# Optimization experiments

Hardware: AMD Instinct MI355X
Metric: run time of the kernel (lower is better)

The kernel has to match this reference:

```python
import jax, jax.numpy as jnp
import numpy as np

B, S, DM, H, DK, R, THETA = 8, 2048, 512, 8, 64, 128, 10000.0
BLK = R          # key/query block size; window radius == block size
NB = S // BLK    # number of blocks
NEG = -1e30      # additive mask for invalid positions (fp32-safe)


def setup_inputs() -> dict:
    key = jax.random.key(0)
    ks = jax.random.split(key, 5)
    scale = 0.02
    hidden_states = jax.random.normal(ks[0], (B, S, DM), jnp.float32)
    Wq = jax.random.normal(ks[1], (DM, H * DK), jnp.float32) * scale
    Wk = jax.random.normal(ks[2], (DM, H * DK), jnp.float32) * scale
    Wv = jax.random.normal(ks[3], (DM, H * DK), jnp.float32) * scale
    Wo = jax.random.normal(ks[4], (H * DK, DM), jnp.float32) * scale
    position_ids = jnp.tile(jnp.arange(S, dtype=jnp.int64)[None, :], (B, 1))
    return {"hidden_states": hidden_states, "Wq": Wq, "Wk": Wk, "Wv": Wv,
            "Wo": Wo, "position_ids": position_ids}


def _apply_rope(q, k, position_ids):
    # q,k: [B,H,S,DK]; position_ids: [B,S]
    half = DK // 2
    inv_freq = 1.0 / (THETA ** (jnp.arange(0, DK, 2, dtype=jnp.float32) / DK))  # [half]
    freqs = position_ids.astype(jnp.float32)[:, :, None] * inv_freq[None, None, :]  # [B,S,half]
    emb = jnp.concatenate([freqs, freqs], axis=-1)        # [B,S,DK]
    cos = jnp.cos(emb)[:, None, :, :]                     # [B,1,S,DK]
    sin = jnp.sin(emb)[:, None, :, :]

    def rotate_half(x):
        return jnp.concatenate([-x[..., half:], x[..., :half]], axis=-1)

    return q * cos + rotate_half(q) * sin, k * cos + rotate_half(k) * sin


def _band_mask():
    # valid[nb, BLK, 3*BLK]: key within [0,S) and |j - i| <= R
    b = jnp.arange(NB)[:, None, None]
    qi = jnp.arange(BLK)[None, :, None]
    kj = jnp.arange(3 * BLK)[None, None, :]
    kglob = (b - 1) * BLK + kj                 # global key index
    qglob = b * BLK + qi                        # global query index
    return (jnp.abs(kglob - qglob) <= R) & (kglob >= 0) & (kglob < S)


def reference(hidden_states, Wq, Wk, Wv, Wo, position_ids):
    # projections: [B,S,DM] -> [B,H,S,DK]
    def shape(x):
        return x.reshape(B, S, H, DK).transpose(0, 2, 1, 3)

    q = shape(hidden_states @ Wq)
    k = shape(hidden_states @ Wk)
    v = shape(hidden_states @ Wv)
    q, k = _apply_rope(q, k, position_ids)

    # block-banded sliding-window attention, softmax_scale = 1.0 (no scaling)
    pad = ((0, 0), (0, 0), (BLK, BLK), (0, 0))
    kb = jnp.pad(k, pad).reshape(B, H, NB + 2, BLK, DK)
    vb = jnp.pad(v, pad).reshape(B, H, NB + 2, BLK, DK)
    # neighbor window: blocks [b-1, b, b+1] -> [B,H,NB,3*BLK,DK]
    kwin = jnp.concatenate([kb[:, :, i:i + NB] for i in range(3)], axis=3)
    vwin = jnp.concatenate([vb[:, :, i:i + NB] for i in range(3)], axis=3)
    qb = q.reshape(B, H, NB, BLK, DK)

    scores = jnp.einsum('bhnqd,bhnkd->bhnqk', qb, kwin)   # unscaled
    valid = _band_mask()                                  # [NB,BLK,3*BLK]
    scores = jnp.where(valid[None, None], scores, NEG)
    attn = jax.nn.softmax(scores.astype(jnp.float32), axis=-1).astype(scores.dtype)
    outb = jnp.einsum('bhnqk,bhnkd->bhnqd', attn, vwin)   # [B,H,NB,BLK,DK]

    out = outb.reshape(B, H, S, DK).transpose(0, 2, 1, 3).reshape(B, S, H * DK)
    return out @ Wo
```

## Files before the change

kernel.cpp:

```cpp
#include <hip/hip_runtime.h>

using bf16 = __bf16;
typedef __bf16 bf16x8 __attribute__((ext_vector_type(8)));
typedef __bf16 bf16x4 __attribute__((ext_vector_type(4)));
typedef float f32x4 __attribute__((ext_vector_type(4)));
typedef float f32x16 __attribute__((ext_vector_type(16)));

#define MFMA16(a, b, c) __builtin_amdgcn_mfma_f32_16x16x32_bf16((a), (b), (c), 0, 0, 0)
#define MFMA32(a, b, c) __builtin_amdgcn_mfma_f32_32x32x16_bf16((a), (b), (c), 0, 0, 0)

constexpr int S = 2048, DM = 512, H = 8, DK = 64, HD = 512;
constexpr int NBLK = 16, BLK = 128;
constexpr int Mrows = 8 * S;
constexpr float LOG2E = 1.44269504088896340736f;

__device__ __forceinline__ void gll16(const void* g, void* l) {
  __builtin_amdgcn_global_load_lds((const __attribute__((address_space(1))) unsigned int*)g,
                                   (__attribute__((address_space(3))) unsigned int*)l, 16, 0, 0);
}

__global__ void k_conv(const float* __restrict__ x, bf16* __restrict__ y) {
  size_t i = ((size_t)blockIdx.x * 256 + threadIdx.x) * 8;
  float4 a = *(const float4*)(x + i);
  float4 b = *(const float4*)(x + i + 4);
  bf16x8 o;
  o[0] = (bf16)a.x; o[1] = (bf16)a.y; o[2] = (bf16)a.z; o[3] = (bf16)a.w;
  o[4] = (bf16)b.x; o[5] = (bf16)b.y; o[6] = (bf16)b.z; o[7] = (bf16)b.w;
  *(bf16x8*)(y + i) = o;
}

__global__ void k_transw4(const float* __restrict__ W0, const float* __restrict__ W1,
                          const float* __restrict__ W2, const float* __restrict__ W3,
                          bf16* __restrict__ D0, bf16* __restrict__ D1,
                          bf16* __restrict__ D2, bf16* __restrict__ D3) {
  const int z = blockIdx.z;
  const float* W = (z == 0) ? W0 : (z == 1) ? W1 : (z == 2) ? W2 : W3;
  bf16* Wt = (z == 0) ? D0 : (z == 1) ? D1 : (z == 2) ? D2 : D3;
  __shared__ float tile[32][33];
  int k0 = blockIdx.x * 32, n0 = blockIdx.y * 32;
  int tx = threadIdx.x, ty = threadIdx.y;
#pragma unroll
  for (int i = 0; i < 4; i++)
    tile[ty * 4 + i][tx] = W[(size_t)(k0 + ty * 4 + i) * 512 + n0 + tx];
  __syncthreads();
#pragma unroll
  for (int i = 0; i < 4; i++)
    Wt[(size_t)(n0 + ty * 4 + i) * 512 + k0 + tx] = (bf16)tile[tx][ty * 4 + i];
}

__global__ void k_ctab(float2* __restrict__ ctab) {
  int idx = blockIdx.x * 256 + threadIdx.x;
  int s = idx >> 5, i = idx & 31;
  float invf = exp2f(-(float)i * (13.287712379549449f / 32.0f));
  float ang = (float)s * invf;
  ctab[idx] = make_float2(cosf(ang), sinf(ang));
}

__global__ __launch_bounds__(256) void k_gemm_qkv(
    const bf16* __restrict__ Xb,
    const bf16* __restrict__ Wtq, const bf16* __restrict__ Wtk, const bf16* __restrict__ Wtv,
    bf16* __restrict__ Qo, bf16* __restrict__ Ko, bf16* __restrict__ Vt,
    const float2* __restrict__ ctab) {
  const int z = blockIdx.z;
  const bf16* Wt = (z == 0) ? Wtq : ((z == 1) ? Wtk : Wtv);
  bf16* dst = (z == 0) ? Qo : Ko;
  const float qscale = (z == 0) ? LOG2E : 1.0f;

  __shared__ __align__(16) char Asm[128 * 64];
  __shared__ __align__(16) char Bsm[128 * 64];

  const int t = threadIdx.x, l = t & 63, wid = t >> 6;
  const int l15 = l & 15, l4 = l >> 4;
  const int wm = wid >> 1, wn = wid & 1;
  const size_t arow0 = (size_t)blockIdx.x * 128;
  const size_t brow0 = (size_t)blockIdx.y * 128;

  f32x4 acc[4][4] = {};
  const int rs = wid * 16 + (l >> 2);
  const int cs = (l & 3) ^ ((l >> 2) & 3);

  for (int kt = 0; kt < 16; ++kt) {
    const int k0 = kt * 32;
    __syncthreads();
    gll16(Xb + (arow0 + rs) * 512 + k0 + cs * 8,      Asm + wid * 1024);
    gll16(Xb + (arow0 + 64 + rs) * 512 + k0 + cs * 8, Asm + 4096 + wid * 1024);
    gll16(Wt + (brow0 + rs) * 512 + k0 + cs * 8,      Bsm + wid * 1024);
    gll16(Wt + (brow0 + 64 + rs) * 512 + k0 + cs * 8, Bsm + 4096 + wid * 1024);
    __syncthreads();
    bf16x8 af[4], bfr[4];
#pragma unroll
    for (int mi = 0; mi < 4; mi++) {
      int row = wm * 64 + mi * 16 + l15;
      af[mi] = *(const bf16x8*)(Asm + row * 64 + ((l4 ^ (row & 3)) * 16));
    }
#pragma unroll
    for (int ni = 0; ni < 4; ni++) {
      int row = wn * 64 + ni * 16 + l15;
      bfr[ni] = *(const bf16x8*)(Bsm + row * 64 + ((l4 ^ (row & 3)) * 16));
    }
#pragma unroll
    for (int mi = 0; mi < 4; mi++)
#pragma unroll
      for (int ni = 0; ni < 4; ni++)
        acc[mi][ni] = MFMA16(af[mi], bfr[ni], acc[mi][ni]);
  }

  if (z == 2) {
    const int b = (int)(arow0 >> 11);
#pragma unroll
    for (int mi = 0; mi < 4; mi++) {
      int scol = (int)(arow0 & 2047) + wm * 64 + mi * 16 + l4 * 4;
#pragma unroll
      for (int ni = 0; ni < 4; ni++) {
        int col = (int)brow0 + wn * 64 + ni * 16 + l15;
        int hh = col >> 6, dd = col & 63;
        bf16x4 pk = {(bf16)acc[mi][ni][0], (bf16)acc[mi][ni][1],
                     (bf16)acc[mi][ni][2], (bf16)acc[mi][ni][3]};
        *(bf16x4*)(Vt + ((size_t)((b * H + hh) * 64 + dd)) * 2048 + scol) = pk;
      }
    }
    return;
  }

#pragma unroll
  for (int mi = 0; mi < 4; mi++) {
#pragma unroll
    for (int r = 0; r < 4; r++) {
      int grow = (int)arow0 + wm * 64 + mi * 16 + l4 * 4 + r;
      size_t rowoff = (size_t)grow * 512 + brow0 + wn * 64;
      int s = grow & (S - 1);
      float2 cs0 = ctab[s * 32 + l15];
      float2 cs1 = ctab[s * 32 + 16 + l15];
#pragma unroll
      for (int ni = 0; ni < 4; ni++) {
        float a = acc[mi][ni][r];
        float b = acc[mi][ni ^ 2][r];
        float2 cc = (ni & 1) ? cs1 : cs0;
        float val = (ni < 2) ? (a * cc.x - b * cc.y) : (a * cc.x + b * cc.y);
        dst[rowoff + ni * 16 + l15] = (bf16)(val * qscale);
      }
    }
  }
}

__global__ __launch_bounds__(256) void k_gemm_out(
    const bf16* __restrict__ A, const bf16* __restrict__ Wt, float* __restrict__ out) {
  __shared__ __align__(16) char Asm[128 * 64];
  __shared__ __align__(16) char Bsm[128 * 64];

  const int t = threadIdx.x, l = t & 63, wid = t >> 6;
  const int l15 = l & 15, l4 = l >> 4;
  const int wm = wid >> 1, wn = wid & 1;
  const size_t arow0 = (size_t)blockIdx.x * 128;
  const size_t brow0 = (size_t)blockIdx.y * 128;

  f32x4 acc[4][4] = {};
  const int rs = wid * 16 + (l >> 2);
  const int cs = (l & 3) ^ ((l >> 2) & 3);

  for (int kt = 0; kt < 16; ++kt) {
    const int k0 = kt * 32;
    __syncthreads();
    gll16(A + (arow0 + rs) * 512 + k0 + cs * 8,       Asm + wid * 1024);
    gll16(A + (arow0 + 64 + rs) * 512 + k0 + cs * 8,  Asm + 4096 + wid * 1024);
    gll16(Wt + (brow0 + rs) * 512 + k0 + cs * 8,      Bsm + wid * 1024);
    gll16(Wt + (brow0 + 64 + rs) * 512 + k0 + cs * 8, Bsm + 4096 + wid * 1024);
    __syncthreads();
    bf16x8 af[4], bfr[4];
#pragma unroll
    for (int mi = 0; mi < 4; mi++) {
      int row = wm * 64 + mi * 16 + l15;
      af[mi] = *(const bf16x8*)(Asm + row * 64 + ((l4 ^ (row & 3)) * 16));
    }
#pragma unroll
    for (int ni = 0; ni < 4; ni++) {
      int row = wn * 64 + ni * 16 + l15;
      bfr[ni] = *(const bf16x8*)(Bsm + row * 64 + ((l4 ^ (row & 3)) * 16));
    }
#pragma unroll
    for (int mi = 0; mi < 4; mi++)
#pragma unroll
      for (int ni = 0; ni < 4; ni++)
        acc[mi][ni] = MFMA16(af[mi], bfr[ni], acc[mi][ni]);
  }

#pragma unroll
  for (int mi = 0; mi < 4; mi++)
#pragma unroll
    for (int r = 0; r < 4; r++) {
      int grow = (int)arow0 + wm * 64 + mi * 16 + l4 * 4 + r;
      size_t rowoff = (size_t)grow * 512 + brow0 + wn * 64;
#pragma unroll
      for (int ni = 0; ni < 4; ni++)
        out[rowoff + ni * 16 + l15] = acc[mi][ni][r];
    }
}

__global__ __launch_bounds__(256) void k_attn(
    const bf16* __restrict__ Q, const bf16* __restrict__ K, const bf16* __restrict__ Vt,
    bf16* __restrict__ O) {
  const int nb = blockIdx.x, h = blockIdx.y, bb = blockIdx.z;
  const int t = threadIdx.x, l = t & 63, w = t >> 6;
  const int q31 = l & 31, hi = l >> 5;

  const int bh = bb * H + h;
  const size_t qrow = (size_t)bb * S + nb * BLK + w * 32 + q31;

  const bf16* Qp = Q + qrow * HD + h * DK + hi * 8;
  bf16x8 qb[4];
#pragma unroll
  for (int ks = 0; ks < 4; ks++) qb[ks] = *(const bf16x8*)(Qp + ks * 16);

  f32x16 o0 = {}, o1 = {};
  float mrun = -3e38f, lrun = 0.f;

  const bf16* Kbase = K + (size_t)bb * S * HD + h * DK + hi * 8;
  const bf16* Vbase = Vt + ((size_t)bh * 64 + q31) * 2048 + hi * 8;

  for (int cr = 0; cr < 9; ++cr) {
    const int kg0 = nb * BLK + (w + cr) * 32 - 128;
    if (kg0 < 0 || kg0 >= S) continue;

    const bf16* Kp = Kbase + (size_t)(kg0 + q31) * HD;
    bf16x8 ka0 = *(const bf16x8*)(Kp);
    bf16x8 ka1 = *(const bf16x8*)(Kp + 16);
    bf16x8 ka2 = *(const bf16x8*)(Kp + 32);
    bf16x8 ka3 = *(const bf16x8*)(Kp + 48);
    const bf16* Vp = Vbase + kg0;
    bf16x8 va00 = *(const bf16x8*)(Vp);
    bf16x8 va01 = *(const bf16x8*)(Vp + 16);
    bf16x8 va10 = *(const bf16x8*)(Vp + 32 * 2048);
    bf16x8 va11 = *(const bf16x8*)(Vp + 32 * 2048 + 16);

    f32x16 acc = {};
    acc = MFMA32(ka0, qb[0], acc);
    acc = MFMA32(ka1, qb[1], acc);
    acc = MFMA32(ka2, qb[2], acc);
    acc = MFMA32(ka3, qb[3], acc);

    if (cr == 0) {
#pragma unroll
      for (int rg = 0; rg < 16; rg++) {
        int kk = (rg & 3) + 8 * (rg >> 2) + 4 * hi;
        if (kk < q31) acc[rg] = -1e30f;
      }
    } else if (cr == 8) {
#pragma unroll
      for (int rg = 0; rg < 16; rg++) {
        int kk = (rg & 3) + 8 * (rg >> 2) + 4 * hi;
        if (kk > q31) acc[rg] = -1e30f;
      }
    }

    float m = acc[0];
#pragma unroll
    for (int rg = 1; rg < 16; rg++) m = fmaxf(m, acc[rg]);
    m = fmaxf(m, __shfl_xor(m, 32));
    const float mnew = fmaxf(mrun, m);
    const float alpha = exp2f(mrun - mnew);
    mrun = mnew;
    float p[16];
    float rs = 0.f;
#pragma unroll
    for (int rg = 0; rg < 16; rg++) {
      p[rg] = exp2f(acc[rg] - mnew);
      rs += p[rg];
    }
    rs += __shfl_xor(rs, 32);
    lrun = lrun * alpha + rs;
#pragma unroll
    for (int rg = 0; rg < 16; rg++) { o0[rg] *= alpha; o1[rg] *= alpha; }

    unsigned int Wd[4][2];
#pragma unroll
    for (int a = 0; a < 4; a++)
#pragma unroll
      for (int b2 = 0; b2 < 2; b2++) {
        unsigned int wd;
        asm("v_cvt_pk_bf16_f32 %0, %1, %2" : "=v"(wd) : "v"(p[4 * a + 2 * b2]), "v"(p[4 * a + 2 * b2 + 1]));
        Wd[a][b2] = wd;
      }
    bf16x8 pf[2];
#pragma unroll
    for (int ks = 0; ks < 2; ks++) {
      union { unsigned int u[4]; bf16x8 v; } cvt;
#pragma unroll
      for (int b2 = 0; b2 < 2; b2++) {
        unsigned int low_w = Wd[2 * ks][b2];
        unsigned int hi_w  = Wd[2 * ks + 1][b2];
        unsigned int msg = hi ? low_w : hi_w;
        unsigned int rec = __shfl_xor(msg, 32);
        cvt.u[b2]     = hi ? rec : low_w;
        cvt.u[2 + b2] = hi ? hi_w : rec;
      }
      pf[ks] = cvt.v;
    }

    o0 = MFMA32(va00, pf[0], o0);
    o0 = MFMA32(va01, pf[1], o0);
    o1 = MFMA32(va10, pf[0], o1);
    o1 = MFMA32(va11, pf[1], o1);
  }

  const float inv = 1.0f / lrun;
  bf16* Op = O + qrow * HD + h * DK + 4 * hi;
#pragma unroll
  for (int dt = 0; dt < 2; dt++) {
    const f32x16 oo = dt ? o1 : o0;
#pragma unroll
    for (int a = 0; a < 4; a++) {
      bf16x4 ob = {(bf16)(oo[4 * a + 0] * inv), (bf16)(oo[4 * a + 1] * inv),
                   (bf16)(oo[4 * a + 2] * inv), (bf16)(oo[4 * a + 3] * inv)};
      *(bf16x4*)(Op + dt * 32 + 8 * a) = ob;
    }
  }
}

extern "C" void kernel_launch(void* const* d_in, const int* in_sizes, int n_in,
                              void* d_out, int out_size, void* d_ws, size_t ws_size,
                              hipStream_t stream) {
  const float* hs = (const float*)d_in[0];
  const float* Wq = (const float*)d_in[1];
  const float* Wk = (const float*)d_in[2];
  const float* Wv = (const float*)d_in[3];
  const float* Wo = (const float*)d_in[4];
  float* out = (float*)d_out;

  char* ws = (char*)d_ws;
  const size_t MB = 1u << 20;
  bf16* Xb = (bf16*)(ws);
  bf16* Qb = (bf16*)(ws + 16 * MB);
  bf16* Kb = (bf16*)(ws + 32 * MB);
  bf16* Vt = (bf16*)(ws + 48 * MB);
  bf16* Wtq = (bf16*)(ws + 64 * MB);
  bf16* Wtk = Wtq + 512 * 512;
  bf16* Wtv = Wtk + 512 * 512;
  bf16* Wto = Wtv + 512 * 512;
  float2* ctab = (float2*)(ws + 64 * MB + 4 * 512 * 512 * sizeof(bf16));
  bf16* AO = Xb;

  k_conv<<<dim3(Mrows * DM / (256 * 8)), dim3(256), 0, stream>>>(hs, Xb);
  k_transw4<<<dim3(16, 16, 4), dim3(32, 8), 0, stream>>>(Wq, Wk, Wv, Wo, Wtq, Wtk, Wtv, Wto);
  k_ctab<<<dim3(S * 32 / 256), dim3(256), 0, stream>>>(ctab);
  k_gemm_qkv<<<dim3(Mrows / 128, 4, 3), dim3(256), 0, stream>>>(Xb, Wtq, Wtk, Wtv, Qb, Kb, Vt, ctab);
  k_attn<<<dim3(NBLK, H, 8), dim3(256), 0, stream>>>(Qb, Kb, Vt, AO);
  k_gemm_out<<<dim3(Mrows / 128, 4), dim3(256), 0, stream>>>(AO, Wto, out);
}
```

Baseline: 124.7 us.

## Pair key chunks per softmax step with lazy rescale and block swizzle

Measured after the change: 117.2 us. -6.0%, faster.

```diff
diff --git a/kernel.cpp b/kernel.cpp
--- a/kernel.cpp
+++ b/kernel.cpp
@@ -196,10 +196,12 @@
     }
 }
 
-__global__ __launch_bounds__(256) void k_attn(
+__global__ __launch_bounds__(256, 4) void k_attn(
     const bf16* __restrict__ Q, const bf16* __restrict__ K, const bf16* __restrict__ Vt,
     bf16* __restrict__ O) {
-  const int nb = blockIdx.x, h = blockIdx.y, bb = blockIdx.z;
+  const int bid = blockIdx.x;
+  const int swz = (bid & 7) * 128 + (bid >> 3);
+  const int nb = swz & 15, h = (swz >> 4) & 7, bb = swz >> 7;
   const int t = threadIdx.x, l = t & 63, w = t >> 6;
   const int q31 = l & 31, hi = l >> 5;
 
@@ -216,61 +218,9 @@
 
   const bf16* Kbase = K + (size_t)bb * S * HD + h * DK + hi * 8;
   const bf16* Vbase = Vt + ((size_t)bh * 64 + q31) * 2048 + hi * 8;
-
-  for (int cr = 0; cr < 9; ++cr) {
-    const int kg0 = nb * BLK + (w + cr) * 32 - 128;
-    if (kg0 < 0 || kg0 >= S) continue;
-
-    const bf16* Kp = Kbase + (size_t)(kg0 + q31) * HD;
-    bf16x8 ka0 = *(const bf16x8*)(Kp);
-    bf16x8 ka1 = *(const bf16x8*)(Kp + 16);
-    bf16x8 ka2 = *(const bf16x8*)(Kp + 32);
-    bf16x8 ka3 = *(const bf16x8*)(Kp + 48);
-    const bf16* Vp = Vbase + kg0;
-    bf16x8 va00 = *(const bf16x8*)(Vp);
-    bf16x8 va01 = *(const bf16x8*)(Vp + 16);
-    bf16x8 va10 = *(const bf16x8*)(Vp + 32 * 2048);
-    bf16x8 va11 = *(const bf16x8*)(Vp + 32 * 2048 + 16);
-
-    f32x16 acc = {};
-    acc = MFMA32(ka0, qb[0], acc);
-    acc = MFMA32(ka1, qb[1], acc);
-    acc = MFMA32(ka2, qb[2], acc);
-    acc = MFMA32(ka3, qb[3], acc);
-
-    if (cr == 0) {
-#pragma unroll
-      for (int rg = 0; rg < 16; rg++) {
-        int kk = (rg & 3) + 8 * (rg >> 2) + 4 * hi;
-        if (kk < q31) acc[rg] = -1e30f;
-      }
-    } else if (cr == 8) {
-#pragma unroll
-      for (int rg = 0; rg < 16; rg++) {
-        int kk = (rg & 3) + 8 * (rg >> 2) + 4 * hi;
-        if (kk > q31) acc[rg] = -1e30f;
-      }
-    }
-
-    float m = acc[0];
-#pragma unroll
-    for (int rg = 1; rg < 16; rg++) m = fmaxf(m, acc[rg]);
-    m = fmaxf(m, __shfl_xor(m, 32));
-    const float mnew = fmaxf(mrun, m);
-    const float alpha = exp2f(mrun - mnew);
-    mrun = mnew;
-    float p[16];
-    float rs = 0.f;
-#pragma unroll
-    for (int rg = 0; rg < 16; rg++) {
-      p[rg] = exp2f(acc[rg] - mnew);
-      rs += p[rg];
-    }
-    rs += __shfl_xor(rs, 32);
-    lrun = lrun * alpha + rs;
-#pragma unroll
-    for (int rg = 0; rg < 16; rg++) { o0[rg] *= alpha; o1[rg] *= alpha; }
-
+  const int s0 = nb * BLK + w * 32 - 128;
+
+  auto pv = [&](const f32x16& p, int kgc) {
     unsigned int Wd[4][2];
 #pragma unroll
     for (int a = 0; a < 4; a++)
@@ -295,11 +245,90 @@
       }
       pf[ks] = cvt.v;
     }
-
-    o0 = MFMA32(va00, pf[0], o0);
-    o0 = MFMA32(va01, pf[1], o0);
-    o1 = MFMA32(va10, pf[0], o1);
-    o1 = MFMA32(va11, pf[1], o1);
+    const bf16* Vp = Vbase + kgc;
+    o0 = MFMA32(*(const bf16x8*)(Vp), pf[0], o0);
+    o0 = MFMA32(*(const bf16x8*)(Vp + 16), pf[1], o0);
+    o1 = MFMA32(*(const bf16x8*)(Vp + 32 * 2048), pf[0], o1);
+    o1 = MFMA32(*(const bf16x8*)(Vp + 32 * 2048 + 16), pf[1], o1);
+  };
+
+#pragma unroll
+  for (int st = 0; st < 5; ++st) {
+    const bool has2 = (st < 4);
+    const int c0 = st * 2, c1 = c0 + 1;
+    const int kg0 = s0 + c0 * 32, kg1 = s0 + c1 * 32;
+    const int kc0 = kg0 < 0 ? 0 : (kg0 > S - 32 ? S - 32 : kg0);
+    const int kc1 = kg1 < 0 ? 0 : (kg1 > S - 32 ? S - 32 : kg1);
+
+    f32x16 a0 = {}, a1 = {};
+    {
+      const bf16* Kp = Kbase + (size_t)(kc0 + q31) * HD;
+      a0 = MFMA32(*(const bf16x8*)(Kp),      qb[0], a0);
+      a0 = MFMA32(*(const bf16x8*)(Kp + 16), qb[1], a0);
+      a0 = MFMA32(*(const bf16x8*)(Kp + 32), qb[2], a0);
+      a0 = MFMA32(*(const bf16x8*)(Kp + 48), qb[3], a0);
+    }
+    if (has2) {
+      const bf16* Kp = Kbase + (size_t)(kc1 + q31) * HD;
+      a1 = MFMA32(*(const bf16x8*)(Kp),      qb[0], a1);
+      a1 = MFMA32(*(const bf16x8*)(Kp + 16), qb[1], a1);
+      a1 = MFMA32(*(const bf16x8*)(Kp + 32), qb[2], a1);
+      a1 = MFMA32(*(const bf16x8*)(Kp + 48), qb[3], a1);
+    }
+
+    if (kg0 != kc0) {
+#pragma unroll
+      for (int rg = 0; rg < 16; rg++) a0[rg] = -1e30f;
+    } else if (c0 == 0) {
+#pragma unroll
+      for (int rg = 0; rg < 16; rg++) {
+        int kk = (rg & 3) + 8 * (rg >> 2) + 4 * hi;
+        if (kk < q31) a0[rg] = -1e30f;
+      }
+    } else if (c0 == 8) {
+#pragma unroll
+      for (int rg = 0; rg < 16; rg++) {
+        int kk = (rg & 3) + 8 * (rg >> 2) + 4 * hi;
+        if (kk > q31) a0[rg] = -1e30f;
+      }
+    }
+    if (has2 && kg1 != kc1) {
+#pragma unroll
+      for (int rg = 0; rg < 16; rg++) a1[rg] = -1e30f;
+    }
+
+    f32x16 mx = a0;
+    if (has2) {
+#pragma unroll
+      for (int rg = 0; rg < 16; rg++) mx[rg] = fmaxf(mx[rg], a1[rg]);
+    }
+#pragma unroll
+    for (int sl = 8; sl >= 1; sl >>= 1)
+#pragma unroll
+      for (int i = 0; i < sl; i++) mx[i] = fmaxf(mx[i], mx[i + sl]);
+    const float pm = fmaxf(mx[0], __shfl_xor(mx[0], 32));
+
+    if (!__all(pm - mrun <= 8.0f)) {
+      const float mnew = fmaxf(mrun, pm);
+      const float alpha = exp2f(mrun - mnew);
+      lrun *= alpha;
+#pragma unroll
+      for (int rg = 0; rg < 16; rg++) { o0[rg] *= alpha; o1[rg] *= alpha; }
+      mrun = mnew;
+    }
+
+    float rsum = 0.f;
+#pragma unroll
+    for (int rg = 0; rg < 16; rg++) { a0[rg] = exp2f(a0[rg] - mrun); rsum += a0[rg]; }
+    if (has2) {
+#pragma unroll
+      for (int rg = 0; rg < 16; rg++) { a1[rg] = exp2f(a1[rg] - mrun); rsum += a1[rg]; }
+    }
+    rsum += __shfl_xor(rsum, 32);
+    lrun += rsum;
+
+    pv(a0, kc0);
+    if (has2) pv(a1, kc1);
   }
 
   const float inv = 1.0f / lrun;
@@ -343,6 +372,6 @@
   k_transw4<<<dim3(16, 16, 4), dim3(32, 8), 0, stream>>>(Wq, Wk, Wv, Wo, Wtq, Wtk, Wtv, Wto);
   k_ctab<<<dim3(S * 32 / 256), dim3(256), 0, stream>>>(ctab);
   k_gemm_qkv<<<dim3(Mrows / 128, 4, 3), dim3(256), 0, stream>>>(Xb, Wtq, Wtk, Wtv, Qb, Kb, Vt, ctab);
-  k_attn<<<dim3(NBLK, H, 8), dim3(256), 0, stream>>>(Qb, Kb, Vt, AO);
+  k_attn<<<dim3(NBLK * H * 8), dim3(256), 0, stream>>>(Qb, Kb, Vt, AO);
   k_gemm_out<<<dim3(Mrows / 128, 4), dim3(256), 0, stream>>>(AO, Wto, out);
 }
```
